# Kernel tuning notes

Hardware: AMD Instinct MI355X
Metric: run time of the kernel (lower is better)

The kernel has to match this reference:

```python
import jax, jax.numpy as jnp
import numpy as np

N = 100_000      # nodes
E = 3_200_000    # edges (avg degree 32)
F_IN = 64        # num_node_features
G = 256          # graphs in batch


def _lin(key, fan_in, fan_out):
    kw, kb = jax.random.split(key)
    bound = 1.0 / np.sqrt(fan_in)
    W = jax.random.uniform(kw, (fan_in, fan_out), jnp.float32, -bound, bound)
    b = jax.random.uniform(kb, (fan_out,), jnp.float32, -bound, bound)
    return W, b


def setup_inputs() -> dict:
    key = jax.random.key(0)
    ks = jax.random.split(key, 9)
    x = jax.random.normal(ks[0], (N, F_IN), jnp.float32)
    edge_index = jax.random.randint(ks[1], (2, E), 0, N, dtype=jnp.int64)
    batch = jnp.sort(jax.random.randint(ks[2], (N,), 0, G, dtype=jnp.int64))
    W1, b1 = _lin(ks[3], F_IN, 60)
    W2, b2 = _lin(ks[4], 60, 50)
    Wf1, bf1 = _lin(ks[5], 50, 30)
    Wf2, bf2 = _lin(ks[6], 30, 20)
    Wf3, bf3 = _lin(ks[7], 20, 10)
    Wo, bo = _lin(ks[8], 10, 1)
    return {"x": x, "edge_index": edge_index, "batch": batch,
            "W1": W1, "b1": b1, "W2": W2, "b2": b2,
            "Wf1": Wf1, "bf1": bf1, "Wf2": Wf2, "bf2": bf2,
            "Wf3": Wf3, "bf3": bf3, "Wo": Wo, "bo": bo}


def _gcn_norm(edge_index, n_nodes):
    # add self loops, then symmetric D^{-1/2} (A+I) D^{-1/2} edge weights
    loop = jnp.arange(n_nodes, dtype=edge_index.dtype)
    src = jnp.concatenate([edge_index[0], loop])
    dst = jnp.concatenate([edge_index[1], loop])
    deg = jax.ops.segment_sum(jnp.ones_like(dst, dtype=jnp.float32), dst,
                              num_segments=n_nodes)
    dinv = jax.lax.rsqrt(deg)  # deg >= 1 thanks to self loops
    norm = dinv[src] * dinv[dst]
    return src, dst, norm


def _gcn_conv(h, W, b, src, dst, norm, n_nodes):
    h = h @ W                                            # [N, out]
    msg = h[src] * norm[:, None]                         # gather over edges
    agg = jax.ops.segment_sum(msg, dst, num_segments=n_nodes)
    return agg + b


def reference(x, edge_index, batch, W1, b1, W2, b2,
              Wf1, bf1, Wf2, bf2, Wf3, bf3, Wo, bo):
    n_nodes = x.shape[0]
    src, dst, norm = _gcn_norm(edge_index, n_nodes)
    h = _gcn_conv(x, W1, b1, src, dst, norm, n_nodes)    # [N, 60]
    h = _gcn_conv(h, W2, b2, src, dst, norm, n_nodes)    # [N, 50]
    # global_add_pool over graph ids
    g = jax.ops.segment_sum(h, batch, num_segments=G)    # [G, 50]
    # MLP stack (no nonlinearities in the original forward)
    g = g @ Wf1 + bf1
    g = g @ Wf2 + bf2
    g = g @ Wf3 + bf3
    return g @ Wo + bo                                   # [G, 1]
```

## Files before the change

### kernel.cpp

```cpp
#include <hip/hip_runtime.h>


#define RSHIFT 7
#define RNODES 128
#define NB_MAX 1024
#define NBLK 512
#define STHREADS 512
#define STAGE_CAP 8192

__device__ __forceinline__ int block_scan_pair(int pair, int tid, int* wsum) {
    int lane = tid & 63, wave = tid >> 6;
    int incl = pair;
    #pragma unroll
    for (int off = 1; off < 64; off <<= 1) {
        int a = __shfl_up(incl, off, 64);
        if (lane >= off) incl += a;
    }
    if (lane == 63) wsum[wave] = incl;
    __syncthreads();
    if (tid < 64) {
        int v = (lane < 8) ? wsum[lane] : 0;
        #pragma unroll
        for (int off = 1; off < 8; off <<= 1) {
            int a = __shfl_up(v, off, 64);
            if (lane >= off) v += a;
        }
        if (lane < 8) wsum[lane] = v;
    }
    __syncthreads();
    int wexcl = wave ? wsum[wave - 1] : 0;
    return wexcl + incl - pair;
}

__global__ void collapse_weights_k(
    const float* __restrict__ W1, const float* __restrict__ b1,
    const float* __restrict__ W2, const float* __restrict__ b2,
    const float* __restrict__ Wf1, const float* __restrict__ bf1,
    const float* __restrict__ Wf2, const float* __restrict__ bf2,
    const float* __restrict__ Wf3, const float* __restrict__ bf3,
    const float* __restrict__ Wo, const float* __restrict__ bo,
    float* __restrict__ w1c, float* __restrict__ sc)
{
    __shared__ float wo[10], w3[20], w2[30], w1[50], w2c[60];
    const int t = threadIdx.x;
    if (t < 10) wo[t] = Wo[t];
    __syncthreads();
    if (t < 20) { float s = 0.f; for (int j = 0; j < 10; ++j) s += Wf3[t*10+j]*wo[j]; w3[t] = s; }
    __syncthreads();
    if (t < 30) { float s = 0.f; for (int j = 0; j < 20; ++j) s += Wf2[t*20+j]*w3[j]; w2[t] = s; }
    __syncthreads();
    if (t < 50) { float s = 0.f; for (int j = 0; j < 30; ++j) s += Wf1[t*30+j]*w2[j]; w1[t] = s; }
    __syncthreads();
    if (t < 60) { float s = 0.f; for (int j = 0; j < 50; ++j) s += W2[t*50+j]*w1[j]; w2c[t] = s; }
    __syncthreads();
    { float s = 0.f; for (int j = 0; j < 60; ++j) s += W1[t*60+j]*w2c[j]; w1c[t] = s; }
    if (t == 0) {
        float c1 = 0.f; for (int j = 0; j < 60; ++j) c1 += b1[j]*w2c[j];
        float c2 = 0.f; for (int j = 0; j < 50; ++j) c2 += b2[j]*w1[j];
        float c0 = bo[0];
        for (int j = 0; j < 30; ++j) c0 += bf1[j]*w2[j];
        for (int j = 0; j < 20; ++j) c0 += bf2[j]*w3[j];
        for (int j = 0; j < 10; ++j) c0 += bf3[j]*wo[j];
        sc[0] = c1; sc[1] = c2; sc[2] = c0;
    }
}

__global__ void node_u_k(const float* __restrict__ x, const float* __restrict__ w1c,
                         float* __restrict__ u, int n) {
    int tid = blockIdx.x * blockDim.x + threadIdx.x;
    int wave = tid >> 6;
    int lane = threadIdx.x & 63;
    int node = wave * 4 + (lane >> 4);
    int sub = lane & 15;
    if (node >= n) return;
    float4 xv = *reinterpret_cast<const float4*>(x + (size_t)node * 64 + sub * 4);
    float4 wv = *reinterpret_cast<const float4*>(w1c + sub * 4);
    float val = xv.x * wv.x + xv.y * wv.y + xv.z * wv.z + xv.w * wv.w;
    val += __shfl_down(val, 8, 16);
    val += __shfl_down(val, 4, 16);
    val += __shfl_down(val, 2, 16);
    val += __shfl_down(val, 1, 16);
    if (sub == 0) u[node] = val;
}

__global__ void __launch_bounds__(STHREADS) bin_count_k(
    const int* __restrict__ dst, int E, int chunk, int nb, int* __restrict__ cnt_bm) {
    __shared__ int hist[NB_MAX];
    int tid = threadIdx.x;
    hist[tid] = 0; hist[tid + 512] = 0;
    __syncthreads();
    int e0 = blockIdx.x * chunk;
    int e1 = e0 + chunk; if (e1 > E) e1 = E;
    for (int i = e0 + tid * 4; i < e1; i += STHREADS * 4) {
        if (i + 3 < e1) {
            int4 d = *reinterpret_cast<const int4*>(dst + i);
            atomicAdd(&hist[d.x >> RSHIFT], 1);
            atomicAdd(&hist[d.y >> RSHIFT], 1);
            atomicAdd(&hist[d.z >> RSHIFT], 1);
            atomicAdd(&hist[d.w >> RSHIFT], 1);
        } else {
            for (int k = i; k < e1; ++k) atomicAdd(&hist[dst[k] >> RSHIFT], 1);
        }
    }
    __syncthreads();
    for (int b = tid; b < nb; b += STHREADS)
        cnt_bm[(size_t)blockIdx.x * nb + b] = hist[b];
}

__global__ void __launch_bounds__(STHREADS) scanA_k(
    const int* __restrict__ cnt_bm, int nb, int* __restrict__ offs, int* __restrict__ total) {
    __shared__ int wsum[8];
    int k = threadIdx.x, b = blockIdx.x;
    int v = cnt_bm[(size_t)k * nb + b];
    int excl = block_scan_pair(v, k, wsum);
    offs[(size_t)b * NBLK + k] = excl;
    if (k == 0) total[b] = wsum[7];
}

__global__ void __launch_bounds__(STHREADS) scanB_k(
    const int* __restrict__ total, int nb, int* __restrict__ base, int* __restrict__ endp,
    const float* __restrict__ sc, float* __restrict__ out, int G) {
    __shared__ int wsum[8];
    int t = threadIdx.x;
    if (t < G) out[t] = sc[2];
    int b0 = 2 * t, b1 = 2 * t + 1;
    int t0 = (b0 < nb) ? total[b0] : 0;
    int t1 = (b1 < nb) ? total[b1] : 0;
    int a0 = (t0 + 3) & ~3, a1 = (t1 + 3) & ~3;
    int excl = block_scan_pair(a0 + a1, t, wsum);
    if (b0 < nb) { base[b0] = excl; endp[b0] = excl + t0; }
    if (b1 < nb) { base[b1] = excl + a0; endp[b1] = excl + a0 + t1; }
}

__global__ void __launch_bounds__(STHREADS) bin_scatter_k(
    const int* __restrict__ src, const int* __restrict__ dst,
    int E, int chunk, int nb,
    const int* __restrict__ base, const int* __restrict__ offs,
    unsigned int* __restrict__ binned) {
    __shared__ unsigned int raw[STAGE_CAP];
    __shared__ unsigned int rb[STAGE_CAP];
    __shared__ unsigned int sorted_[STAGE_CAP];
    __shared__ unsigned short bofs[STAGE_CAP];
    __shared__ int hist[NB_MAX];
    __shared__ int tbase[NB_MAX];
    __shared__ int adj[NB_MAX];
    __shared__ int wsum[8];
    const int tid = threadIdx.x;
    hist[tid] = 0; hist[tid + 512] = 0;
    __syncthreads();
    int e0 = blockIdx.x * chunk;
    int e1 = e0 + chunk; if (e1 > E) e1 = E;
    int tcount = e1 - e0;
    for (int i = e0 + tid * 4; i < e1; i += STHREADS * 4) {
        if (i + 3 < e1) {
            int4 s4 = *reinterpret_cast<const int4*>(src + i);
            int4 d4 = *reinterpret_cast<const int4*>(dst + i);
            int li = i - e0;
            int b, r;
            b = d4.x >> RSHIFT; r = atomicAdd(&hist[b], 1);
            raw[li+0] = (unsigned)s4.x | ((unsigned)(d4.x & (RNODES-1)) << 17);
            rb[li+0] = ((unsigned)b << 16) | (unsigned)r;
            b = d4.y >> RSHIFT; r = atomicAdd(&hist[b], 1);
            raw[li+1] = (unsigned)s4.y | ((unsigned)(d4.y & (RNODES-1)) << 17);
            rb[li+1] = ((unsigned)b << 16) | (unsigned)r;
            b = d4.z >> RSHIFT; r = atomicAdd(&hist[b], 1);
            raw[li+2] = (unsigned)s4.z | ((unsigned)(d4.z & (RNODES-1)) << 17);
            rb[li+2] = ((unsigned)b << 16) | (unsigned)r;
            b = d4.w >> RSHIFT; r = atomicAdd(&hist[b], 1);
            raw[li+3] = (unsigned)s4.w | ((unsigned)(d4.w & (RNODES-1)) << 17);
            rb[li+3] = ((unsigned)b << 16) | (unsigned)r;
        } else {
            for (int k = i; k < e1; ++k) {
                int s = src[k], d = dst[k];
                int b = d >> RSHIFT;
                int r = atomicAdd(&hist[b], 1);
                raw[k - e0] = (unsigned)s | ((unsigned)(d & (RNODES-1)) << 17);
                rb[k - e0] = ((unsigned)b << 16) | (unsigned)r;
            }
        }
    }
    __syncthreads();
    int h0 = hist[2*tid], h1 = hist[2*tid+1];
    int excl = block_scan_pair(h0 + h1, tid, wsum);
    tbase[2*tid] = excl;
    tbase[2*tid+1] = excl + h0;
    __syncthreads();
    {
        int b0 = 2*tid, b1 = 2*tid + 1;
        if (b0 < nb) adj[b0] = base[b0] + offs[(size_t)b0 * NBLK + blockIdx.x] - tbase[b0];
        if (b1 < nb) adj[b1] = base[b1] + offs[(size_t)b1 * NBLK + blockIdx.x] - tbase[b1];
    }
    __syncthreads();
    for (int li = tid; li < tcount; li += STHREADS) {
        unsigned v = rb[li];
        int b = (int)(v >> 16);
        int slot = tbase[b] + (int)(v & 0xFFFF);
        sorted_[slot] = raw[li];
        bofs[slot] = (unsigned short)b;
    }
    __syncthreads();
    for (int s = tid; s < tcount; s += STHREADS) {
        binned[adj[bofs[s]] + s] = sorted_[s];
    }
}

__global__ void __launch_bounds__(STHREADS) degree_k(
    const unsigned int* __restrict__ binned, const int* __restrict__ base,
    const int* __restrict__ endp, const float* __restrict__ u,
    float* __restrict__ dinv, float* __restrict__ w, int n) {
    __shared__ int cnt[RNODES];
    int tid = threadIdx.x, b = blockIdx.x;
    if (tid < RNODES) cnt[tid] = 0;
    __syncthreads();
    int s0 = base[b], s1 = endp[b];
    int nvec = (s1 - s0) >> 2;
    for (int k = tid; k < nvec; k += blockDim.x) {
        uint4 p = *reinterpret_cast<const uint4*>(binned + s0 + 4 * k);
        atomicAdd(&cnt[p.x >> 17], 1);
        atomicAdd(&cnt[p.y >> 17], 1);
        atomicAdd(&cnt[p.z >> 17], 1);
        atomicAdd(&cnt[p.w >> 17], 1);
    }
    int i = s0 + 4 * nvec + tid;
    if (i < s1) atomicAdd(&cnt[binned[i] >> 17], 1);
    __syncthreads();
    int g = (b << RSHIFT) + tid;
    if (tid < RNODES && g < n) {
        float d = rsqrtf((float)(cnt[tid] + 1));
        dinv[g] = d;
        w[g] = d * u[g];
    }
}

__global__ void __launch_bounds__(STHREADS) conv_mid_k(
    const unsigned int* __restrict__ binned, const int* __restrict__ base,
    const int* __restrict__ endp,
    const float* __restrict__ w, const float* __restrict__ dinv,
    const float* __restrict__ u, const float* __restrict__ sc,
    float* __restrict__ v, float* __restrict__ wb, int n) {
    __shared__ float acc[RNODES];
    int tid = threadIdx.x, b = blockIdx.x;
    if (tid < RNODES) acc[tid] = 0.f;
    __syncthreads();
    int s0 = base[b], s1 = endp[b];
    int nvec = (s1 - s0) >> 2;
    for (int k = tid; k < nvec; k += blockDim.x) {
        uint4 p = *reinterpret_cast<const uint4*>(binned + s0 + 4 * k);
        float wx = w[p.x & 0x1FFFF];
        float wy = w[p.y & 0x1FFFF];
        float wz = w[p.z & 0x1FFFF];
        float ww = w[p.w & 0x1FFFF];
        atomicAdd(&acc[p.x >> 17], wx);
        atomicAdd(&acc[p.y >> 17], wy);
        atomicAdd(&acc[p.z >> 17], wz);
        atomicAdd(&acc[p.w >> 17], ww);
    }
    int i = s0 + 4 * nvec + tid;
    if (i < s1) { unsigned p = binned[i]; atomicAdd(&acc[p >> 17], w[p & 0x1FFFF]); }
    __syncthreads();
    int g = (b << RSHIFT) + tid;
    if (tid < RNODES && g < n) {
        float di = dinv[g];
        float val = sc[0] + di * acc[tid] + di * di * u[g];
        v[g] = val;
        wb[g] = di * val;
    }
}

__global__ void __launch_bounds__(STHREADS) conv_final_k(
    const unsigned int* __restrict__ binned, const int* __restrict__ base,
    const int* __restrict__ endp,
    const float* __restrict__ wb, const float* __restrict__ dinv,
    const float* __restrict__ v, const float* __restrict__ sc,
    const int* __restrict__ batch, float* __restrict__ out, int n) {
    __shared__ float acc[RNODES];
    __shared__ float tbuf[RNODES];
    __shared__ int gbuf[RNODES];
    int tid = threadIdx.x, b = blockIdx.x;
    if (tid < RNODES) acc[tid] = 0.f;
    __syncthreads();
    int s0 = base[b], s1 = endp[b];
    int nvec = (s1 - s0) >> 2;
    for (int k = tid; k < nvec; k += blockDim.x) {
        uint4 p = *reinterpret_cast<const uint4*>(binned + s0 + 4 * k);
        float wx = wb[p.x & 0x1FFFF];
        float wy = wb[p.y & 0x1FFFF];
        float wz = wb[p.z & 0x1FFFF];
        float ww = wb[p.w & 0x1FFFF];
        atomicAdd(&acc[p.x >> 17], wx);
        atomicAdd(&acc[p.y >> 17], wy);
        atomicAdd(&acc[p.z >> 17], wz);
        atomicAdd(&acc[p.w >> 17], ww);
    }
    int i = s0 + 4 * nvec + tid;
    if (i < s1) { unsigned p = binned[i]; atomicAdd(&acc[p >> 17], wb[p & 0x1FFFF]); }
    __syncthreads();
    int g = (b << RSHIFT) + tid;
    float tval = 0.f; int gid = -1;
    if (tid < RNODES && g < n) {
        float di = dinv[g];
        tval = sc[1] + di * acc[tid] + di * di * v[g];
        gid = batch[g];
    }
    if (tid < RNODES) { tbuf[tid] = tval; gbuf[tid] = gid; }
    __syncthreads();
    if (tid < RNODES && g < n) {
        bool head = (tid == 0) || (gbuf[tid - 1] != gid);
        if (head) {
            float s = 0.f;
            int i2 = tid;
            while (i2 < RNODES && gbuf[i2] == gid) { s += tbuf[i2]; ++i2; }
            atomicAdd(&out[gid], s);
        }
    }
}

extern "C" void kernel_launch(void* const* d_in, const int* in_sizes, int n_in,
                              void* d_out, int out_size, void* d_ws, size_t ws_size,
                              hipStream_t stream)
{
    const float* x    = (const float*)d_in[0];
    const int*   ei   = (const int*)d_in[1];
    const int*   batch= (const int*)d_in[2];
    const float* W1   = (const float*)d_in[3];
    const float* b1   = (const float*)d_in[4];
    const float* W2   = (const float*)d_in[5];
    const float* b2   = (const float*)d_in[6];
    const float* Wf1  = (const float*)d_in[7];
    const float* bf1  = (const float*)d_in[8];
    const float* Wf2  = (const float*)d_in[9];
    const float* bf2  = (const float*)d_in[10];
    const float* Wf3  = (const float*)d_in[11];
    const float* bf3  = (const float*)d_in[12];
    const float* Wo   = (const float*)d_in[13];
    const float* bo   = (const float*)d_in[14];
    float* out = (float*)d_out;

    const int n = in_sizes[0] / 64;
    const int E = in_sizes[1] / 2;
    const int G = out_size;
    const int* src = ei;
    const int* dst = ei + E;
    const int nb = (n + RNODES - 1) >> RSHIFT;

    float* ws_f = (float*)d_ws;
    int*   ws_i = (int*)d_ws;
    float* w1c    = ws_f;
    float* sc     = ws_f + 64;
    int*   basep  = ws_i + 128;
    int*   endp   = ws_i + 128 + NB_MAX;
    int*   total  = ws_i + 128 + 2*NB_MAX;
    int*   offs   = ws_i + 128 + 3*NB_MAX;
    size_t off_u  = 128 + 3*(size_t)NB_MAX + (size_t)nb * NBLK;
    off_u = (off_u + 3) & ~(size_t)3;
    float* u      = ws_f + off_u;
    float* dinv   = u + n;
    float* w      = dinv + n;
    float* v      = w + n;
    float* wb     = v + n;
    size_t off_b  = off_u + 5*(size_t)n;
    off_b = (off_b + 3) & ~(size_t)3;
    unsigned int* binned = (unsigned int*)(ws_f + off_b);
    int* cnt_bm = (int*)binned;

    int chunk = (E + NBLK - 1) / NBLK;
    chunk = (chunk + 3) & ~3;

    hipLaunchKernelGGL(collapse_weights_k, dim3(1), dim3(64), 0, stream,
                       W1, b1, W2, b2, Wf1, bf1, Wf2, bf2, Wf3, bf3, Wo, bo, w1c, sc);
    hipLaunchKernelGGL(node_u_k, dim3((n / 4 * 64 + 255) / 256 + 1), dim3(256), 0, stream,
                       x, w1c, u, n);
    hipLaunchKernelGGL(bin_count_k, dim3(NBLK), dim3(STHREADS), 0, stream,
                       dst, E, chunk, nb, cnt_bm);
    hipLaunchKernelGGL(scanA_k, dim3(nb), dim3(STHREADS), 0, stream,
                       cnt_bm, nb, offs, total);
    hipLaunchKernelGGL(scanB_k, dim3(1), dim3(STHREADS), 0, stream,
                       total, nb, basep, endp, sc, out, G);
    hipLaunchKernelGGL(bin_scatter_k, dim3(NBLK), dim3(STHREADS), 0, stream,
                       src, dst, E, chunk, nb, basep, offs, binned);
    hipLaunchKernelGGL(degree_k, dim3(nb), dim3(STHREADS), 0, stream,
                       binned, basep, endp, u, dinv, w, n);
    hipLaunchKernelGGL(conv_mid_k, dim3(nb), dim3(STHREADS), 0, stream,
                       binned, basep, endp, w, dinv, u, sc, v, wb, n);
    hipLaunchKernelGGL(conv_final_k, dim3(nb), dim3(STHREADS), 0, stream,
                       binned, basep, endp, wb, dinv, v, sc, batch, out, n);
}
```

Measured before the change: 209.0 us.

## Shrink edge tiles for binning and fuse node projection into degree kernel

Edge binning now uses fixed 4096-edge tiles, so the grid grows from 512 blocks to about 782, the shared staging per block shrinks, and occupancy in the count and scatter passes goes up. The count matrix is transposed to bin-major so scanA reads contiguously, and each thread scans two tiles. The separate node_u kernel is removed; the x·w1c projection is computed inside the degree kernel, one block per bin, which saves a launch and a pass over u. The trade-off is more per-tile offset entries to scan and write, plus extra work in the degree kernel.

```diff
diff --git a/kernel.cpp b/kernel.cpp
--- a/kernel.cpp
+++ b/kernel.cpp
@@ -4,9 +4,8 @@
 #define RSHIFT 7
 #define RNODES 128
 #define NB_MAX 1024
-#define NBLK 512
+#define TILE 4096
 #define STHREADS 512
-#define STAGE_CAP 8192
 
 __device__ __forceinline__ int block_scan_pair(int pair, int tid, int* wsum) {
     int lane = tid & 63, wave = tid >> 6;
@@ -65,33 +64,15 @@
     }
 }
 
-__global__ void node_u_k(const float* __restrict__ x, const float* __restrict__ w1c,
-                         float* __restrict__ u, int n) {
-    int tid = blockIdx.x * blockDim.x + threadIdx.x;
-    int wave = tid >> 6;
-    int lane = threadIdx.x & 63;
-    int node = wave * 4 + (lane >> 4);
-    int sub = lane & 15;
-    if (node >= n) return;
-    float4 xv = *reinterpret_cast<const float4*>(x + (size_t)node * 64 + sub * 4);
-    float4 wv = *reinterpret_cast<const float4*>(w1c + sub * 4);
-    float val = xv.x * wv.x + xv.y * wv.y + xv.z * wv.z + xv.w * wv.w;
-    val += __shfl_down(val, 8, 16);
-    val += __shfl_down(val, 4, 16);
-    val += __shfl_down(val, 2, 16);
-    val += __shfl_down(val, 1, 16);
-    if (sub == 0) u[node] = val;
-}
-
-__global__ void __launch_bounds__(STHREADS) bin_count_k(
-    const int* __restrict__ dst, int E, int chunk, int nb, int* __restrict__ cnt_bm) {
+__global__ void __launch_bounds__(256) bin_count_k(
+    const int* __restrict__ dst, int E, int nb, int NT, int* __restrict__ cnt_bm) {
     __shared__ int hist[NB_MAX];
-    int tid = threadIdx.x;
-    hist[tid] = 0; hist[tid + 512] = 0;
-    __syncthreads();
-    int e0 = blockIdx.x * chunk;
-    int e1 = e0 + chunk; if (e1 > E) e1 = E;
-    for (int i = e0 + tid * 4; i < e1; i += STHREADS * 4) {
+    int tid = threadIdx.x, k = blockIdx.x;
+    for (int b = tid; b < nb; b += 256) hist[b] = 0;
+    __syncthreads();
+    int e0 = k * TILE;
+    int e1 = e0 + TILE; if (e1 > E) e1 = E;
+    for (int i = e0 + tid * 4; i < e1; i += 256 * 4) {
         if (i + 3 < e1) {
             int4 d = *reinterpret_cast<const int4*>(dst + i);
             atomicAdd(&hist[d.x >> RSHIFT], 1);
@@ -99,22 +80,25 @@
             atomicAdd(&hist[d.z >> RSHIFT], 1);
             atomicAdd(&hist[d.w >> RSHIFT], 1);
         } else {
-            for (int k = i; k < e1; ++k) atomicAdd(&hist[dst[k] >> RSHIFT], 1);
-        }
-    }
-    __syncthreads();
-    for (int b = tid; b < nb; b += STHREADS)
-        cnt_bm[(size_t)blockIdx.x * nb + b] = hist[b];
+            for (int q = i; q < e1; ++q) atomicAdd(&hist[dst[q] >> RSHIFT], 1);
+        }
+    }
+    __syncthreads();
+    for (int b = tid; b < nb; b += 256)
+        cnt_bm[(size_t)b * NT + k] = hist[b];
 }
 
 __global__ void __launch_bounds__(STHREADS) scanA_k(
-    const int* __restrict__ cnt_bm, int nb, int* __restrict__ offs, int* __restrict__ total) {
+    const int* __restrict__ cnt_bm, int NT, int* __restrict__ offs, int* __restrict__ total) {
     __shared__ int wsum[8];
-    int k = threadIdx.x, b = blockIdx.x;
-    int v = cnt_bm[(size_t)k * nb + b];
-    int excl = block_scan_pair(v, k, wsum);
-    offs[(size_t)b * NBLK + k] = excl;
-    if (k == 0) total[b] = wsum[7];
+    int t = threadIdx.x, b = blockIdx.x;
+    int k0 = 2 * t, k1 = 2 * t + 1;
+    int v0 = (k0 < NT) ? cnt_bm[(size_t)b * NT + k0] : 0;
+    int v1 = (k1 < NT) ? cnt_bm[(size_t)b * NT + k1] : 0;
+    int excl = block_scan_pair(v0 + v1, t, wsum);
+    if (k0 < NT) offs[(size_t)b * NT + k0] = excl;
+    if (k1 < NT) offs[(size_t)b * NT + k1] = excl + v0;
+    if (t == 0) total[b] = wsum[7];
 }
 
 __global__ void __launch_bounds__(STHREADS) scanB_k(
@@ -134,13 +118,13 @@
 
 __global__ void __launch_bounds__(STHREADS) bin_scatter_k(
     const int* __restrict__ src, const int* __restrict__ dst,
-    int E, int chunk, int nb,
+    int E, int nb, int NT,
     const int* __restrict__ base, const int* __restrict__ offs,
     unsigned int* __restrict__ binned) {
-    __shared__ unsigned int raw[STAGE_CAP];
-    __shared__ unsigned int rb[STAGE_CAP];
-    __shared__ unsigned int sorted_[STAGE_CAP];
-    __shared__ unsigned short bofs[STAGE_CAP];
+    __shared__ unsigned int raw[TILE];
+    __shared__ unsigned int rb[TILE];
+    __shared__ unsigned int sorted_[TILE];
+    __shared__ unsigned short bofs[TILE];
     __shared__ int hist[NB_MAX];
     __shared__ int tbase[NB_MAX];
     __shared__ int adj[NB_MAX];
@@ -148,8 +132,8 @@
     const int tid = threadIdx.x;
     hist[tid] = 0; hist[tid + 512] = 0;
     __syncthreads();
-    int e0 = blockIdx.x * chunk;
-    int e1 = e0 + chunk; if (e1 > E) e1 = E;
+    int e0 = blockIdx.x * TILE;
+    int e1 = e0 + TILE; if (e1 > E) e1 = E;
     int tcount = e1 - e0;
     for (int i = e0 + tid * 4; i < e1; i += STHREADS * 4) {
         if (i + 3 < e1) {
@@ -170,12 +154,12 @@
             raw[li+3] = (unsigned)s4.w | ((unsigned)(d4.w & (RNODES-1)) << 17);
             rb[li+3] = ((unsigned)b << 16) | (unsigned)r;
         } else {
-            for (int k = i; k < e1; ++k) {
-                int s = src[k], d = dst[k];
+            for (int q = i; q < e1; ++q) {
+                int s = src[q], d = dst[q];
                 int b = d >> RSHIFT;
                 int r = atomicAdd(&hist[b], 1);
-                raw[k - e0] = (unsigned)s | ((unsigned)(d & (RNODES-1)) << 17);
-                rb[k - e0] = ((unsigned)b << 16) | (unsigned)r;
+                raw[q - e0] = (unsigned)s | ((unsigned)(d & (RNODES-1)) << 17);
+                rb[q - e0] = ((unsigned)b << 16) | (unsigned)r;
             }
         }
     }
@@ -187,8 +171,8 @@
     __syncthreads();
     {
         int b0 = 2*tid, b1 = 2*tid + 1;
-        if (b0 < nb) adj[b0] = base[b0] + offs[(size_t)b0 * NBLK + blockIdx.x] - tbase[b0];
-        if (b1 < nb) adj[b1] = base[b1] + offs[(size_t)b1 * NBLK + blockIdx.x] - tbase[b1];
+        if (b0 < nb) adj[b0] = base[b0] + offs[(size_t)b0 * NT + blockIdx.x] - tbase[b0];
+        if (b1 < nb) adj[b1] = base[b1] + offs[(size_t)b1 * NT + blockIdx.x] - tbase[b1];
     }
     __syncthreads();
     for (int li = tid; li < tcount; li += STHREADS) {
@@ -204,17 +188,36 @@
     }
 }
 
-__global__ void __launch_bounds__(STHREADS) degree_k(
+__global__ void __launch_bounds__(STHREADS) degree_u_k(
+    const float* __restrict__ x, const float* __restrict__ w1c,
     const unsigned int* __restrict__ binned, const int* __restrict__ base,
-    const int* __restrict__ endp, const float* __restrict__ u,
-    float* __restrict__ dinv, float* __restrict__ w, int n) {
+    const int* __restrict__ endp,
+    float* __restrict__ u, float* __restrict__ dinv, float* __restrict__ w, int n) {
+    __shared__ float u_lds[RNODES];
     __shared__ int cnt[RNODES];
     int tid = threadIdx.x, b = blockIdx.x;
+    int nl = tid >> 2;
+    int quarter = tid & 3;
+    int g0 = (b << RSHIFT) + nl;
+    float val = 0.f;
+    if (g0 < n) {
+        const float* xr = x + (size_t)g0 * 64 + quarter * 16;
+        const float* wr = w1c + quarter * 16;
+        #pragma unroll
+        for (int j = 0; j < 4; ++j) {
+            float4 xv = *reinterpret_cast<const float4*>(xr + 4 * j);
+            float4 wv = *reinterpret_cast<const float4*>(wr + 4 * j);
+            val += xv.x * wv.x + xv.y * wv.y + xv.z * wv.z + xv.w * wv.w;
+        }
+    }
+    val += __shfl_down(val, 2, 4);
+    val += __shfl_down(val, 1, 4);
+    if (quarter == 0) u_lds[nl] = val;
     if (tid < RNODES) cnt[tid] = 0;
     __syncthreads();
     int s0 = base[b], s1 = endp[b];
     int nvec = (s1 - s0) >> 2;
-    for (int k = tid; k < nvec; k += blockDim.x) {
+    for (int k = tid; k < nvec; k += STHREADS) {
         uint4 p = *reinterpret_cast<const uint4*>(binned + s0 + 4 * k);
         atomicAdd(&cnt[p.x >> 17], 1);
         atomicAdd(&cnt[p.y >> 17], 1);
@@ -227,8 +230,10 @@
     int g = (b << RSHIFT) + tid;
     if (tid < RNODES && g < n) {
         float d = rsqrtf((float)(cnt[tid] + 1));
+        float uv = u_lds[tid];
         dinv[g] = d;
-        w[g] = d * u[g];
+        u[g] = uv;
+        w[g] = d * uv;
     }
 }
 
@@ -244,7 +249,7 @@
     __syncthreads();
     int s0 = base[b], s1 = endp[b];
     int nvec = (s1 - s0) >> 2;
-    for (int k = tid; k < nvec; k += blockDim.x) {
+    for (int k = tid; k < nvec; k += STHREADS) {
         uint4 p = *reinterpret_cast<const uint4*>(binned + s0 + 4 * k);
         float wx = w[p.x & 0x1FFFF];
         float wy = w[p.y & 0x1FFFF];
@@ -281,7 +286,7 @@
     __syncthreads();
     int s0 = base[b], s1 = endp[b];
     int nvec = (s1 - s0) >> 2;
-    for (int k = tid; k < nvec; k += blockDim.x) {
+    for (int k = tid; k < nvec; k += STHREADS) {
         uint4 p = *reinterpret_cast<const uint4*>(binned + s0 + 4 * k);
         float wx = wb[p.x & 0x1FFFF];
         float wy = wb[p.y & 0x1FFFF];
@@ -342,6 +347,7 @@
     const int* src = ei;
     const int* dst = ei + E;
     const int nb = (n + RNODES - 1) >> RSHIFT;
+    const int NT = (E + TILE - 1) / TILE;
 
     float* ws_f = (float*)d_ws;
     int*   ws_i = (int*)d_ws;
@@ -351,7 +357,7 @@
     int*   endp   = ws_i + 128 + NB_MAX;
     int*   total  = ws_i + 128 + 2*NB_MAX;
     int*   offs   = ws_i + 128 + 3*NB_MAX;
-    size_t off_u  = 128 + 3*(size_t)NB_MAX + (size_t)nb * NBLK;
+    size_t off_u  = 128 + 3*(size_t)NB_MAX + (size_t)nb * NT;
     off_u = (off_u + 3) & ~(size_t)3;
     float* u      = ws_f + off_u;
     float* dinv   = u + n;
@@ -363,23 +369,18 @@
     unsigned int* binned = (unsigned int*)(ws_f + off_b);
     int* cnt_bm = (int*)binned;
 
-    int chunk = (E + NBLK - 1) / NBLK;
-    chunk = (chunk + 3) & ~3;
-
     hipLaunchKernelGGL(collapse_weights_k, dim3(1), dim3(64), 0, stream,
                        W1, b1, W2, b2, Wf1, bf1, Wf2, bf2, Wf3, bf3, Wo, bo, w1c, sc);
-    hipLaunchKernelGGL(node_u_k, dim3((n / 4 * 64 + 255) / 256 + 1), dim3(256), 0, stream,
-                       x, w1c, u, n);
-    hipLaunchKernelGGL(bin_count_k, dim3(NBLK), dim3(STHREADS), 0, stream,
-                       dst, E, chunk, nb, cnt_bm);
+    hipLaunchKernelGGL(bin_count_k, dim3(NT), dim3(256), 0, stream,
+                       dst, E, nb, NT, cnt_bm);
     hipLaunchKernelGGL(scanA_k, dim3(nb), dim3(STHREADS), 0, stream,
-                       cnt_bm, nb, offs, total);
+                       cnt_bm, NT, offs, total);
     hipLaunchKernelGGL(scanB_k, dim3(1), dim3(STHREADS), 0, stream,
                        total, nb, basep, endp, sc, out, G);
-    hipLaunchKernelGGL(bin_scatter_k, dim3(NBLK), dim3(STHREADS), 0, stream,
-                       src, dst, E, chunk, nb, basep, offs, binned);
-    hipLaunchKernelGGL(degree_k, dim3(nb), dim3(STHREADS), 0, stream,
-                       binned, basep, endp, u, dinv, w, n);
+    hipLaunchKernelGGL(bin_scatter_k, dim3(NT), dim3(STHREADS), 0, stream,
+                       src, dst, E, nb, NT, basep, offs, binned);
+    hipLaunchKernelGGL(degree_u_k, dim3(nb), dim3(STHREADS), 0, stream,
+                       x, w1c, binned, basep, endp, u, dinv, w, n);
     hipLaunchKernelGGL(conv_mid_k, dim3(nb), dim3(STHREADS), 0, stream,
                        binned, basep, endp, w, dinv, u, sc, v, wb, n);
     hipLaunchKernelGGL(conv_final_k, dim3(nb), dim3(STHREADS), 0, stream,
```

After: 210.3 us. No clear change (+0.6%).
